# Optimization experiments

Hardware: AMD Instinct MI355X
Metric: run time of the kernel (lower is better)

## Reference

```python
import jax, jax.numpy as jnp
import numpy as np

N_NODES = 50000
N_EDGES = 800000
D_IN = 64
D_RADIAL = 128


def setup_inputs() -> dict:
    key = jax.random.key(0)
    k1, k2, k3, k4, k5 = jax.random.split(key, 5)
    x = jax.random.normal(k1, (N_NODES, D_IN), dtype=jnp.float32)
    edge_basis = jax.random.normal(k2, (N_EDGES, D_RADIAL), dtype=jnp.float32)
    src = jax.random.randint(k3, (N_EDGES,), 0, N_NODES, dtype=jnp.int32)
    dst = jax.random.randint(k4, (N_EDGES,), 0, N_NODES, dtype=jnp.int32)
    # kaiming normal fan_in, linear nonlinearity: std = 1/sqrt(fan_in)
    W = jax.random.normal(k5, (D_IN, D_RADIAL), dtype=jnp.float32) / jnp.sqrt(
        jnp.float32(D_RADIAL))
    b = jnp.zeros((D_IN,), dtype=jnp.float32)
    return {"x": x, "edge_basis": edge_basis, "src": src, "dst": dst,
            "W": W, "b": b}


def reference(x, edge_basis, src, dst, W, b):
    # per-edge radial filter: Linear(d_radial -> d_in)  [E, d_in]
    filt = jnp.einsum('er,dr->ed', edge_basis, W) + b
    # gather source node features, multiply by filter  [E, d_in]
    m = x[src] * filt
    # scatter-sum messages into destination nodes      [N, d_in]
    h = jax.ops.segment_sum(m, dst, num_segments=x.shape[0])
    return h
```

## Files before the change

### kernel.cpp

```cpp
#include <hip/hip_runtime.h>

#define N_NODES  50000
#define N_EDGES  800000
#define D_IN     64
#define D_RADIAL 128
#define NTILES   (N_EDGES / 64)

typedef __bf16 bf16x8 __attribute__((ext_vector_type(8)));
typedef float  f32x4  __attribute__((ext_vector_type(4)));
typedef short  s16x8  __attribute__((ext_vector_type(8)));

__device__ inline unsigned int pack_bf16_pair(float lo, float hi) {
    return __builtin_amdgcn_perm(__float_as_uint(hi), __float_as_uint(lo), 0x07060302u);
}

__device__ inline unsigned short f2bf_rne(float f) {
    unsigned int u = __float_as_uint(f);
    u += 0x7FFFu + ((u >> 16) & 1u);
    return (unsigned short)(u >> 16);
}

constexpr size_t ws_align(size_t x) { return (x + 255) & ~(size_t)255; }
constexpr size_t WS_CNT  = 0;
constexpr size_t WS_OFF  = ws_align(WS_CNT  + (size_t)N_NODES * 4);
constexpr size_t WS_CUR  = ws_align(WS_OFF  + (size_t)(N_NODES + 1) * 4);
constexpr size_t WS_BSUM = ws_align(WS_CUR  + (size_t)N_NODES * 4);
constexpr size_t WS_ORD  = ws_align(WS_BSUM + 512);
constexpr size_t WS_MSG  = ws_align(WS_ORD  + (size_t)N_EDGES * 4);
constexpr size_t WS_REQUIRED = WS_MSG + (size_t)N_EDGES * D_IN * 2;

#define SCAN_B    512
#define SCAN_NBLK ((N_NODES + SCAN_B - 1) / SCAN_B)
static_assert(SCAN_NBLK <= 128, "scan_tops assumes <=128 blocks");

__global__ __launch_bounds__(256) void hist_kernel(const int* __restrict__ dst,
                                                   int* __restrict__ cnt) {
    int i = blockIdx.x * 256 + threadIdx.x;
    if (i < N_EDGES) atomicAdd(&cnt[dst[i]], 1);
}

__global__ __launch_bounds__(SCAN_B) void scan_block(const int* __restrict__ cnt,
                                                     int* __restrict__ offs,
                                                     int* __restrict__ bsum) {
    const int t = threadIdx.x, b = blockIdx.x;
    const int i = b * SCAN_B + t;
    int v = (i < N_NODES) ? cnt[i] : 0;
    __shared__ int s[SCAN_B];
    s[t] = v;
    __syncthreads();
    for (int o = 1; o < SCAN_B; o <<= 1) {
        int add = (t >= o) ? s[t - o] : 0;
        __syncthreads();
        s[t] += add;
        __syncthreads();
    }
    if (i < N_NODES) offs[i] = s[t];
    if (t == SCAN_B - 1) bsum[b] = s[t];
}

__global__ __launch_bounds__(128) void scan_tops(int* __restrict__ bsum) {
    const int t = threadIdx.x;
    __shared__ int s[128];
    int v = (t < SCAN_NBLK) ? bsum[t] : 0;
    s[t] = v;
    __syncthreads();
    for (int o = 1; o < 128; o <<= 1) {
        int add = (t >= o) ? s[t - o] : 0;
        __syncthreads();
        s[t] += add;
        __syncthreads();
    }
    if (t < SCAN_NBLK) bsum[t] = s[t] - v;
}

__global__ __launch_bounds__(SCAN_B) void finalize_off(const int* __restrict__ cnt,
                                                       int* __restrict__ offs,
                                                       const int* __restrict__ bsum,
                                                       int* __restrict__ cur) {
    const int i = blockIdx.x * SCAN_B + threadIdx.x;
    if (i < N_NODES) {
        int e = offs[i] - cnt[i] + bsum[blockIdx.x];
        offs[i] = e;
        cur[i]  = e;
    }
    if (i == 0) offs[N_NODES] = N_EDGES;
}

__global__ __launch_bounds__(256) void scatter_order(const int* __restrict__ dst,
                                                     int* __restrict__ cur,
                                                     int* __restrict__ order) {
    int i = blockIdx.x * 256 + threadIdx.x;
    if (i < N_EDGES) order[atomicAdd(&cur[dst[i]], 1)] = i;
}

__global__ __launch_bounds__(256) void msg_kernel(
    const float* __restrict__ x,
    const float* __restrict__ eb,
    const int*   __restrict__ src,
    const float* __restrict__ W,
    const float* __restrict__ bias_p,
    unsigned short* __restrict__ msg)
{
    const int lane = threadIdx.x & 63;
    const int wv   = threadIdx.x >> 6;
    const int l15  = lane & 15;
    const int quad = lane >> 4;

    bf16x8 wfrag[4][4];
    #pragma unroll
    for (int nt = 0; nt < 4; ++nt) {
        const int d = nt * 16 + l15;
        #pragma unroll
        for (int kt = 0; kt < 4; ++kt) {
            const float* p = W + d * D_RADIAL + kt * 32 + quad * 8;
            s16x8 s;
            #pragma unroll
            for (int j = 0; j < 8; ++j) s[j] = (short)f2bf_rne(p[j]);
            wfrag[nt][kt] = __builtin_bit_cast(bf16x8, s);
        }
    }
    float bv[4];
    #pragma unroll
    for (int nt = 0; nt < 4; ++nt) bv[nt] = bias_p[nt * 16 + l15];

    for (int tile = blockIdx.x; tile < NTILES; tile += gridDim.x) {
        const int ebase = tile * 64 + wv * 16;
        const int erow  = ebase + quad * 4;

        int sv[4];
        #pragma unroll
        for (int reg = 0; reg < 4; ++reg) sv[reg] = src[erow + reg];

        f32x4 acc[4];
        #pragma unroll
        for (int nt = 0; nt < 4; ++nt) acc[nt] = (f32x4){0.f, 0.f, 0.f, 0.f};

        #pragma unroll
        for (int kt = 0; kt < 4; ++kt) {
            const float* p = eb + (long)(ebase + l15) * D_RADIAL + kt * 32 + quad * 8;
            f32x4 a0 = *(const f32x4*)(p);
            f32x4 a1 = *(const f32x4*)(p + 4);
            int4 packed;
            packed.x = pack_bf16_pair(a0[0], a0[1]);
            packed.y = pack_bf16_pair(a0[2], a0[3]);
            packed.z = pack_bf16_pair(a1[0], a1[1]);
            packed.w = pack_bf16_pair(a1[2], a1[3]);
            bf16x8 afrag = __builtin_bit_cast(bf16x8, packed);
            #pragma unroll
            for (int nt = 0; nt < 4; ++nt)
                acc[nt] = __builtin_amdgcn_mfma_f32_16x16x32_bf16(
                    afrag, wfrag[nt][kt], acc[nt], 0, 0, 0);
        }

        #pragma unroll
        for (int reg = 0; reg < 4; ++reg) {
            const float*    xrow = x   + (long)sv[reg] * D_IN;
            unsigned short* mrow = msg + (long)(erow + reg) * D_IN;
            #pragma unroll
            for (int nt = 0; nt < 4; ++nt) {
                const int d = nt * 16 + l15;
                __builtin_nontemporal_store(
                    f2bf_rne((acc[nt][reg] + bv[nt]) * xrow[d]), mrow + d);
            }
        }
    }
}

__global__ __launch_bounds__(256) void gather_out(
    const unsigned short* __restrict__ msg,
    const int* __restrict__ order,
    const int* __restrict__ offs,
    float* __restrict__ out)
{
    const int lane = threadIdx.x & 63;
    const int wid  = blockIdx.x * 4 + (threadIdx.x >> 6);
    const int wstr = gridDim.x * 4;
    for (int n = wid; n < N_NODES; n += wstr) {
        const int j0 = offs[n], j1 = offs[n + 1];
        float a0 = 0.f, a1 = 0.f, a2 = 0.f, a3 = 0.f;
        int j = j0;
        for (; j + 4 <= j1; j += 4) {
            const long r0 = order[j],     r1 = order[j + 1];
            const long r2 = order[j + 2], r3 = order[j + 3];
            a0 += __uint_as_float((unsigned int)msg[r0 * D_IN + lane] << 16);
            a1 += __uint_as_float((unsigned int)msg[r1 * D_IN + lane] << 16);
            a2 += __uint_as_float((unsigned int)msg[r2 * D_IN + lane] << 16);
            a3 += __uint_as_float((unsigned int)msg[r3 * D_IN + lane] << 16);
        }
        for (; j < j1; ++j)
            a0 += __uint_as_float((unsigned int)msg[(long)order[j] * D_IN + lane] << 16);
        out[(size_t)n * D_IN + lane] = (a0 + a1) + (a2 + a3);
    }
}

__global__ __launch_bounds__(256) void edge_msg_kernel(
    const float* __restrict__ x,
    const float* __restrict__ eb,
    const int*   __restrict__ src,
    const int*   __restrict__ dst,
    const float* __restrict__ W,
    const float* __restrict__ bias_p,
    float*       __restrict__ out)
{
    const int lane = threadIdx.x & 63;
    const int wv   = threadIdx.x >> 6;
    const int l15  = lane & 15;
    const int quad = lane >> 4;

    bf16x8 wfrag[4][4];
    #pragma unroll
    for (int nt = 0; nt < 4; ++nt) {
        const int d = nt * 16 + l15;
        #pragma unroll
        for (int kt = 0; kt < 4; ++kt) {
            const float* p = W + d * D_RADIAL + kt * 32 + quad * 8;
            s16x8 s;
            #pragma unroll
            for (int j = 0; j < 8; ++j) s[j] = (short)f2bf_rne(p[j]);
            wfrag[nt][kt] = __builtin_bit_cast(bf16x8, s);
        }
    }
    float bv[4];
    #pragma unroll
    for (int nt = 0; nt < 4; ++nt) bv[nt] = bias_p[nt * 16 + l15];

    for (int tile = blockIdx.x; tile < NTILES; tile += gridDim.x) {
        const int ebase = tile * 64 + wv * 16;

        f32x4 acc[4];
        #pragma unroll
        for (int nt = 0; nt < 4; ++nt) acc[nt] = (f32x4){0.f, 0.f, 0.f, 0.f};

        #pragma unroll
        for (int kt = 0; kt < 4; ++kt) {
            const float* p = eb + (long)(ebase + l15) * D_RADIAL + kt * 32 + quad * 8;
            f32x4 a0 = *(const f32x4*)(p);
            f32x4 a1 = *(const f32x4*)(p + 4);
            int4 packed;
            packed.x = pack_bf16_pair(a0[0], a0[1]);
            packed.y = pack_bf16_pair(a0[2], a0[3]);
            packed.z = pack_bf16_pair(a1[0], a1[1]);
            packed.w = pack_bf16_pair(a1[2], a1[3]);
            bf16x8 afrag = __builtin_bit_cast(bf16x8, packed);
            #pragma unroll
            for (int nt = 0; nt < 4; ++nt)
                acc[nt] = __builtin_amdgcn_mfma_f32_16x16x32_bf16(
                    afrag, wfrag[nt][kt], acc[nt], 0, 0, 0);
        }

        const int erow = ebase + quad * 4;
        #pragma unroll
        for (int reg = 0; reg < 4; ++reg) {
            const int e  = erow + reg;
            const int sv = src[e];
            const int dv = dst[e];
            const float* xrow = x   + (long)sv * D_IN;
            float*       orow = out + (long)dv * D_IN;
            #pragma unroll
            for (int nt = 0; nt < 4; ++nt) {
                const int d = nt * 16 + l15;
                const float val = (acc[nt][reg] + bv[nt]) * xrow[d];
                unsafeAtomicAdd(orow + d, val);
            }
        }
    }
}

extern "C" void kernel_launch(void* const* d_in, const int* in_sizes, int n_in,
                              void* d_out, int out_size, void* d_ws, size_t ws_size,
                              hipStream_t stream) {
    const float* x    = (const float*)d_in[0];
    const float* eb   = (const float*)d_in[1];
    const int*   src  = (const int*)d_in[2];
    const int*   dst  = (const int*)d_in[3];
    const float* W    = (const float*)d_in[4];
    const float* bias = (const float*)d_in[5];
    float* out = (float*)d_out;

    if (ws_size >= WS_REQUIRED) {
        char* ws   = (char*)d_ws;
        int*  cnt  = (int*)(ws + WS_CNT);
        int*  offs = (int*)(ws + WS_OFF);
        int*  cur  = (int*)(ws + WS_CUR);
        int*  bsum = (int*)(ws + WS_BSUM);
        int*  order = (int*)(ws + WS_ORD);
        unsigned short* msg = (unsigned short*)(ws + WS_MSG);

        hipMemsetAsync(cnt, 0, (size_t)N_NODES * 4, stream);
        hist_kernel   <<<(N_EDGES + 255) / 256, 256, 0, stream>>>(dst, cnt);
        scan_block    <<<SCAN_NBLK, SCAN_B, 0, stream>>>(cnt, offs, bsum);
        scan_tops     <<<1, 128, 0, stream>>>(bsum);
        finalize_off  <<<SCAN_NBLK, SCAN_B, 0, stream>>>(cnt, offs, bsum, cur);
        scatter_order <<<(N_EDGES + 255) / 256, 256, 0, stream>>>(dst, cur, order);
        msg_kernel    <<<1280, 256, 0, stream>>>(x, eb, src, W, bias, msg);
        gather_out    <<<1024, 256, 0, stream>>>(msg, order, offs, out);
    } else {
        hipMemsetAsync(d_out, 0, (size_t)N_NODES * D_IN * sizeof(float), stream);
        edge_msg_kernel<<<1024, 256, 0, stream>>>(x, eb, src, dst, W, bias, out);
    }
}
```

Measured before the change: 752.0 us.

## Fuse message computation into per-node CSR gather, eliminating message buffer

Replaces the two-pass scheme, which wrote bf16 per-edge messages and then gathered them per destination node, with a single node-centric kernel. Each wavefront walks a node's incoming edges in 16-edge MFMA tiles, computes filter times x[src] and reduces directly into the output row. The sorted src indices are materialised alongside the edge order during the scatter build. This removes the large intermediate message write and read, at the cost of gathered edge_basis row reads and wasted MFMA lanes on partially filled tiles for low-degree nodes.

```diff
diff --git a/kernel.cpp b/kernel.cpp
--- a/kernel.cpp
+++ b/kernel.cpp
@@ -25,9 +25,9 @@
 constexpr size_t WS_OFF  = ws_align(WS_CNT  + (size_t)N_NODES * 4);
 constexpr size_t WS_CUR  = ws_align(WS_OFF  + (size_t)(N_NODES + 1) * 4);
 constexpr size_t WS_BSUM = ws_align(WS_CUR  + (size_t)N_NODES * 4);
-constexpr size_t WS_ORD  = ws_align(WS_BSUM + 512);
-constexpr size_t WS_MSG  = ws_align(WS_ORD  + (size_t)N_EDGES * 4);
-constexpr size_t WS_REQUIRED = WS_MSG + (size_t)N_EDGES * D_IN * 2;
+constexpr size_t WS_EORD = ws_align(WS_BSUM + 512);
+constexpr size_t WS_SSRC = ws_align(WS_EORD + (size_t)N_EDGES * 4);
+constexpr size_t WS_REQUIRED = WS_SSRC + (size_t)N_EDGES * 4;
 
 #define SCAN_B    512
 #define SCAN_NBLK ((N_NODES + SCAN_B - 1) / SCAN_B)
@@ -86,20 +86,28 @@
     if (i == 0) offs[N_NODES] = N_EDGES;
 }
 
-__global__ __launch_bounds__(256) void scatter_order(const int* __restrict__ dst,
+__global__ __launch_bounds__(256) void scatter_build(const int* __restrict__ dst,
+                                                     const int* __restrict__ src,
                                                      int* __restrict__ cur,
-                                                     int* __restrict__ order) {
+                                                     int* __restrict__ eord,
+                                                     int* __restrict__ ssrc) {
     int i = blockIdx.x * 256 + threadIdx.x;
-    if (i < N_EDGES) order[atomicAdd(&cur[dst[i]], 1)] = i;
-}
-
-__global__ __launch_bounds__(256) void msg_kernel(
+    if (i < N_EDGES) {
+        int pos = atomicAdd(&cur[dst[i]], 1);
+        eord[pos] = i;
+        ssrc[pos] = src[i];
+    }
+}
+
+__global__ __launch_bounds__(256) void node_kernel(
     const float* __restrict__ x,
     const float* __restrict__ eb,
-    const int*   __restrict__ src,
+    const int*   __restrict__ eord,
+    const int*   __restrict__ ssrc,
+    const int*   __restrict__ offs,
     const float* __restrict__ W,
     const float* __restrict__ bias_p,
-    unsigned short* __restrict__ msg)
+    float*       __restrict__ out)
 {
     const int lane = threadIdx.x & 63;
     const int wv   = threadIdx.x >> 6;
@@ -123,73 +131,71 @@
     #pragma unroll
     for (int nt = 0; nt < 4; ++nt) bv[nt] = bias_p[nt * 16 + l15];
 
-    for (int tile = blockIdx.x; tile < NTILES; tile += gridDim.x) {
-        const int ebase = tile * 64 + wv * 16;
-        const int erow  = ebase + quad * 4;
-
-        int sv[4];
-        #pragma unroll
-        for (int reg = 0; reg < 4; ++reg) sv[reg] = src[erow + reg];
-
-        f32x4 acc[4];
-        #pragma unroll
-        for (int nt = 0; nt < 4; ++nt) acc[nt] = (f32x4){0.f, 0.f, 0.f, 0.f};
-
-        #pragma unroll
-        for (int kt = 0; kt < 4; ++kt) {
-            const float* p = eb + (long)(ebase + l15) * D_RADIAL + kt * 32 + quad * 8;
-            f32x4 a0 = *(const f32x4*)(p);
-            f32x4 a1 = *(const f32x4*)(p + 4);
-            int4 packed;
-            packed.x = pack_bf16_pair(a0[0], a0[1]);
-            packed.y = pack_bf16_pair(a0[2], a0[3]);
-            packed.z = pack_bf16_pair(a1[0], a1[1]);
-            packed.w = pack_bf16_pair(a1[2], a1[3]);
-            bf16x8 afrag = __builtin_bit_cast(bf16x8, packed);
+    const int wid = blockIdx.x * 4 + wv;
+    const int nw  = gridDim.x * 4;
+    for (int n = wid; n < N_NODES; n += nw) {
+        const int j0 = offs[n], j1 = offs[n + 1];
+
+        float nacc[4] = {0.f, 0.f, 0.f, 0.f};
+
+        for (int p0 = j0; p0 < j1; p0 += 16) {
+            const int  pA = p0 + l15;
+            const bool av = (pA < j1);
+            const int  e  = eord[av ? pA : (j1 - 1)];
+
+            f32x4 acc[4];
+            #pragma unroll
+            for (int nt = 0; nt < 4; ++nt) acc[nt] = (f32x4){0.f, 0.f, 0.f, 0.f};
+
+            #pragma unroll
+            for (int kt = 0; kt < 4; ++kt) {
+                bf16x8 afrag;
+                if (av) {
+                    const float* p = eb + (long)e * D_RADIAL + kt * 32 + quad * 8;
+                    f32x4 a0 = *(const f32x4*)(p);
+                    f32x4 a1 = *(const f32x4*)(p + 4);
+                    int4 packed;
+                    packed.x = pack_bf16_pair(a0[0], a0[1]);
+                    packed.y = pack_bf16_pair(a0[2], a0[3]);
+                    packed.z = pack_bf16_pair(a1[0], a1[1]);
+                    packed.w = pack_bf16_pair(a1[2], a1[3]);
+                    afrag = __builtin_bit_cast(bf16x8, packed);
+                } else {
+                    afrag = __builtin_bit_cast(bf16x8, (int4){0, 0, 0, 0});
+                }
+                #pragma unroll
+                for (int nt = 0; nt < 4; ++nt)
+                    acc[nt] = __builtin_amdgcn_mfma_f32_16x16x32_bf16(
+                        afrag, wfrag[nt][kt], acc[nt], 0, 0, 0);
+            }
+
+            #pragma unroll
+            for (int reg = 0; reg < 4; ++reg) {
+                const int  row = quad * 4 + reg;
+                const int  pos = p0 + row;
+                const bool rv  = (pos < j1);
+                const int  s   = ssrc[rv ? pos : (j1 - 1)];
+                const float* xrow = x + (long)s * D_IN;
+                #pragma unroll
+                for (int nt = 0; nt < 4; ++nt) {
+                    const float xv  = xrow[nt * 16 + l15];
+                    const float val = (acc[nt][reg] + bv[nt]) * xv;
+                    nacc[nt] += rv ? val : 0.f;
+                }
+            }
+        }
+
+        #pragma unroll
+        for (int nt = 0; nt < 4; ++nt) {
+            nacc[nt] += __shfl_xor(nacc[nt], 16, 64);
+            nacc[nt] += __shfl_xor(nacc[nt], 32, 64);
+        }
+        if (quad == 0) {
+            float* orow = out + (size_t)n * D_IN;
             #pragma unroll
             for (int nt = 0; nt < 4; ++nt)
-                acc[nt] = __builtin_amdgcn_mfma_f32_16x16x32_bf16(
-                    afrag, wfrag[nt][kt], acc[nt], 0, 0, 0);
-        }
-
-        #pragma unroll
-        for (int reg = 0; reg < 4; ++reg) {
-            const float*    xrow = x   + (long)sv[reg] * D_IN;
-            unsigned short* mrow = msg + (long)(erow + reg) * D_IN;
-            #pragma unroll
-            for (int nt = 0; nt < 4; ++nt) {
-                const int d = nt * 16 + l15;
-                __builtin_nontemporal_store(
-                    f2bf_rne((acc[nt][reg] + bv[nt]) * xrow[d]), mrow + d);
-            }
-        }
-    }
-}
-
-__global__ __launch_bounds__(256) void gather_out(
-    const unsigned short* __restrict__ msg,
-    const int* __restrict__ order,
-    const int* __restrict__ offs,
-    float* __restrict__ out)
-{
-    const int lane = threadIdx.x & 63;
-    const int wid  = blockIdx.x * 4 + (threadIdx.x >> 6);
-    const int wstr = gridDim.x * 4;
-    for (int n = wid; n < N_NODES; n += wstr) {
-        const int j0 = offs[n], j1 = offs[n + 1];
-        float a0 = 0.f, a1 = 0.f, a2 = 0.f, a3 = 0.f;
-        int j = j0;
-        for (; j + 4 <= j1; j += 4) {
-            const long r0 = order[j],     r1 = order[j + 1];
-            const long r2 = order[j + 2], r3 = order[j + 3];
-            a0 += __uint_as_float((unsigned int)msg[r0 * D_IN + lane] << 16);
-            a1 += __uint_as_float((unsigned int)msg[r1 * D_IN + lane] << 16);
-            a2 += __uint_as_float((unsigned int)msg[r2 * D_IN + lane] << 16);
-            a3 += __uint_as_float((unsigned int)msg[r3 * D_IN + lane] << 16);
-        }
-        for (; j < j1; ++j)
-            a0 += __uint_as_float((unsigned int)msg[(long)order[j] * D_IN + lane] << 16);
-        out[(size_t)n * D_IN + lane] = (a0 + a1) + (a2 + a3);
+                orow[nt * 16 + l15] = nacc[nt];
+        }
     }
 }
 
@@ -283,17 +289,16 @@
         int*  offs = (int*)(ws + WS_OFF);
         int*  cur  = (int*)(ws + WS_CUR);
         int*  bsum = (int*)(ws + WS_BSUM);
-        int*  order = (int*)(ws + WS_ORD);
-        unsigned short* msg = (unsigned short*)(ws + WS_MSG);
+        int*  eord = (int*)(ws + WS_EORD);
+        int*  ssrc = (int*)(ws + WS_SSRC);
 
         hipMemsetAsync(cnt, 0, (size_t)N_NODES * 4, stream);
         hist_kernel   <<<(N_EDGES + 255) / 256, 256, 0, stream>>>(dst, cnt);
         scan_block    <<<SCAN_NBLK, SCAN_B, 0, stream>>>(cnt, offs, bsum);
         scan_tops     <<<1, 128, 0, stream>>>(bsum);
         finalize_off  <<<SCAN_NBLK, SCAN_B, 0, stream>>>(cnt, offs, bsum, cur);
-        scatter_order <<<(N_EDGES + 255) / 256, 256, 0, stream>>>(dst, cur, order);
-        msg_kernel    <<<1280, 256, 0, stream>>>(x, eb, src, W, bias, msg);
-        gather_out    <<<1024, 256, 0, stream>>>(msg, order, offs, out);
+        scatter_build <<<(N_EDGES + 255) / 256, 256, 0, stream>>>(dst, src, cur, eord, ssrc);
+        node_kernel   <<<1280, 256, 0, stream>>>(x, eb, eord, ssrc, offs, W, bias, out);
     } else {
         hipMemsetAsync(d_out, 0, (size_t)N_NODES * D_IN * sizeof(float), stream);
         edge_msg_kernel<<<1024, 256, 0, stream>>>(x, eb, src, dst, W, bias, out);
```

New measurement: 775.6 us. +3.1%, slower.
